# Performance work log

Measured on AMD Instinct MI355X. Metric: run time of the kernel, lower is better.

Reference implementation:

```python
import jax, jax.numpy as jnp
import numpy as np
from jax import lax

NPOINT = 1024   # num_points (FPS centroids)
RADIUS = 0.2    # ball-query radius
K = 32          # samples per ball
FILTERS = [64, 64, 128]


def setup_inputs() -> dict:
    key = jax.random.key(0)
    ks = jax.random.split(key, 10)
    B, N, C = 16, 4096, 64
    xyz = jax.random.uniform(ks[0], (B, N, 3), dtype=jnp.float32)   # unit-cube cloud
    points = jax.random.normal(ks[1], (B, N, C), dtype=jnp.float32)
    inp = {"xyz": xyz, "points": points}
    cin = C + 3  # use_xyz=True concatenates relative xyz
    for i, f in enumerate(FILTERS):
        scale = np.sqrt(2.0 / (cin + f)).astype(np.float32)  # glorot_normal
        inp[f"w{i}"] = jax.random.normal(ks[2 + i], (cin, f), dtype=jnp.float32) * scale
        inp[f"b{i}"] = jnp.zeros((f,), dtype=jnp.float32)
        cin = f
    return inp


def farthest_point_sample(xyz, npoint):
    # Serial greedy FPS. xyz: [B,N,3] -> idx [B,npoint] int32
    B, N, _ = xyz.shape

    def body(carry, _):
        dist, far = carry                                   # [B,N], [B]
        centroid = jnp.take_along_axis(xyz, far[:, None, None], axis=1)  # [B,1,3]
        d = jnp.sum((xyz - centroid) ** 2, axis=-1)         # [B,N]
        dist = jnp.minimum(dist, d)
        nxt = jnp.argmax(dist, axis=-1).astype(jnp.int32)
        return (dist, nxt), far

    init = (jnp.full((B, N), 1e10, xyz.dtype), jnp.zeros((B,), jnp.int32))
    _, idxs = lax.scan(body, init, None, length=npoint)
    return idxs.T  # [B,npoint]


def query_ball(radius, nsample, xyz, new_xyz):
    # First-nsample-in-order points within radius; pad with first hit (CUDA semantics).
    B, N, _ = xyz.shape
    d2 = jnp.sum((new_xyz[:, :, None, :] - xyz[:, None, :, :]) ** 2, axis=-1)  # [B,S,N]
    mask = d2 <= radius * radius
    order = jnp.where(mask, jnp.arange(N, dtype=jnp.int32)[None, None, :], N)
    idx_sorted = jnp.sort(order, axis=-1)[..., :nsample]    # first K valid indices
    first = idx_sorted[..., :1]
    first = jnp.where(first < N, first, 0)                  # empty-ball fallback
    return jnp.where(idx_sorted < N, idx_sorted, first)     # [B,S,K]


def reference(xyz, points, w0, b0, w1, b1, w2, b2):
    B, N, _ = xyz.shape
    fps_idx = farthest_point_sample(xyz, NPOINT)                    # [B,S]
    new_xyz = jnp.take_along_axis(xyz, fps_idx[:, :, None], axis=1)  # [B,S,3]
    idx = query_ball(RADIUS, K, xyz, new_xyz)                        # [B,S,K]

    bix = jnp.arange(B)[:, None, None]
    grouped_xyz = xyz[bix, idx] - new_xyz[:, :, None, :]             # [B,S,K,3] recentered
    grouped_pts = points[bix, idx]                                   # [B,S,K,C]
    g = jnp.concatenate([grouped_pts, grouped_xyz], axis=-1)         # [B,S,K,C+3]

    for w, b in ((w0, b0), (w1, b1), (w2, b2)):                      # shared 1x1-conv MLP
        g = jax.nn.relu(jnp.einsum('bskc,cf->bskf', g, w) + b)
    new_points = jnp.max(g, axis=2)                                  # max-pool over ball
    return new_xyz, new_points
```

## Files before the change

### kernel.cpp

```cpp
#include <hip/hip_runtime.h>
#include <stdint.h>

#define BB 16
#define NN 4096
#define CC 64
#define NPOINT 1024
#define KK 32
#define F1 64
#define F2 64
#define F3 128

#define FPS_T 512
#define PPT (NN / FPS_T)

typedef float v2f __attribute__((ext_vector_type(2)));

#if defined(__has_builtin)
#if __has_builtin(__builtin_amdgcn_update_dpp)
#define HAS_DPP 1
#endif
#endif

#ifdef HAS_DPP
template <int CTRL>
__device__ __forceinline__ unsigned long long dpp_move64(unsigned long long k) {
    int lo = __builtin_amdgcn_update_dpp(0, (int)(unsigned)k,         CTRL, 0xF, 0xF, false);
    int hi = __builtin_amdgcn_update_dpp(0, (int)(unsigned)(k >> 32), CTRL, 0xF, 0xF, false);
    return ((unsigned long long)(unsigned)hi << 32) | (unsigned)lo;
}
__device__ __forceinline__ unsigned long long wave_max_key(unsigned long long key) {
    unsigned long long o;
    o = dpp_move64<0x111>(key); if (o > key) key = o;
    o = dpp_move64<0x112>(key); if (o > key) key = o;
    o = dpp_move64<0x114>(key); if (o > key) key = o;
    o = dpp_move64<0x118>(key); if (o > key) key = o;
    o = dpp_move64<0x142>(key); if (o > key) key = o;
    o = dpp_move64<0x143>(key); if (o > key) key = o;
    return key;
}
#else
__device__ __forceinline__ unsigned long long wave_max_key(unsigned long long key) {
#pragma unroll
    for (int off = 32; off > 0; off >>= 1) {
        unsigned long long o = __shfl_xor(key, off, 64);
        if (o > key) key = o;
    }
    return key;
}
#endif

#define SMEM_BYTES 49664

__global__ __launch_bounds__(512)
void fused_kernel(const float* __restrict__ xyz,
                  const float* __restrict__ points,
                  const float* __restrict__ w0, const float* __restrict__ b0,
                  const float* __restrict__ w1, const float* __restrict__ b1,
                  const float* __restrict__ w2, const float* __restrict__ b2,
                  float* __restrict__ out_xyz,
                  float* __restrict__ out_points,
                  int* __restrict__ ctr) {
    __shared__ __align__(16) char smem[SMEM_BYTES];
    const int tid = threadIdx.x;

    if (blockIdx.x < BB) {
        asm volatile("s_setprio 3");
        float* xs = (float*)smem;
        float* ys = xs + NN;
        float* zs = ys + NN;
        unsigned long long (*wred)[FPS_T / 64] =
            (unsigned long long (*)[FPS_T / 64])(smem + 49152);
        float* cbuf = (float*)(smem + 49280);

        const int b = blockIdx.x;
        const int lane = tid & 63, wid = tid >> 6;
        const float* __restrict__ xb = xyz + (size_t)b * (NN * 3);

        v2f px2[4], py2[4], pz2[4], dd[4];
#pragma unroll
        for (int j = 0; j < 4; ++j) {
#pragma unroll
            for (int h = 0; h < 2; ++h) {
                int p = tid + (2 * j + h) * FPS_T;
                float x = xb[p * 3 + 0];
                float y = xb[p * 3 + 1];
                float z = xb[p * 3 + 2];
                px2[j][h] = x; py2[j][h] = y; pz2[j][h] = z;
                xs[p] = x; ys[p] = y; zs[p] = z;
            }
            dd[j] = (v2f){1e10f, 1e10f};
        }
        __syncthreads();

        float cx = xs[0], cy = ys[0], cz = zs[0];
        float* xo = out_xyz + (size_t)b * NPOINT * 3;

        for (int i = 0; i < NPOINT; ++i) {
            if (tid == 0) {
                cbuf[(i & 31) * 3 + 0] = cx;
                cbuf[(i & 31) * 3 + 1] = cy;
                cbuf[(i & 31) * 3 + 2] = cz;
            }
            {
#pragma clang fp contract(off)
                v2f c2x = (v2f){cx, cx}, c2y = (v2f){cy, cy}, c2z = (v2f){cz, cz};
#pragma unroll
                for (int j = 0; j < 4; ++j) {
                    v2f dx = px2[j] - c2x;
                    v2f dy = py2[j] - c2y;
                    v2f dz = pz2[j] - c2z;
                    v2f ss = (dx * dx + dy * dy) + dz * dz;
                    dd[j] = __builtin_elementwise_min(dd[j], ss);
                }
            }
            v2f m01 = __builtin_elementwise_max(dd[0], dd[1]);
            v2f m23 = __builtin_elementwise_max(dd[2], dd[3]);
            v2f mm  = __builtin_elementwise_max(m01, m23);
            float bd = fmaxf(mm.x, mm.y);
            int bp = 0;
#pragma unroll
            for (int j = 3; j >= 0; --j) {
                if (dd[j].y == bd) bp = tid + (2 * j + 1) * FPS_T;
                if (dd[j].x == bd) bp = tid + (2 * j + 0) * FPS_T;
            }
            unsigned long long key = (((unsigned long long)__float_as_uint(bd)) << 32)
                                   | (unsigned int)(NN - 1 - bp);
            key = wave_max_key(key);
            if (lane == 63) wred[i & 1][wid] = key;
            __syncthreads();

            unsigned long long best = wred[i & 1][0];
#pragma unroll
            for (int w = 1; w < FPS_T / 64; ++w) {
                unsigned long long o = wred[i & 1][w];
                if (o > best) best = o;
            }
            int bi = (NN - 1) - (int)(best & 0xffffffffu);

            if (tid == 0 && (i & 31) == 31) {
                const float4* src = (const float4*)cbuf;
                float4* dst = (float4*)(xo + (size_t)(i - 31) * 3);
#pragma unroll
                for (int q = 0; q < 24; ++q) dst[q] = src[q];
                __hip_atomic_store(&ctr[b * 16], i + 1,
                                   __ATOMIC_RELEASE, __HIP_MEMORY_SCOPE_AGENT);
            }
            cx = xs[bi]; cy = ys[bi]; cz = zs[bi];
        }
    } else {
        float (*gbuf)[68] = (float (*)[68])smem;
        float (*hbuf)[F1] = (float (*)[F1])(smem + 8704);
        float (*pmax)[F3] = (float (*)[F3])(smem + 16896);
        unsigned long long* cmask = (unsigned long long*)(smem + 20992);
        int* nbr = (int*)(smem + 21504);

        const int gi = blockIdx.x - BB;
        const int s = gi >> 4;
        const int b = gi & 15;
        const int g = b * NPOINT + s;
        const int f = tid & 63;
        const int wid = tid >> 6;

        if (tid == 0) {
            const int target = s + 1;
            int c;
            while ((c = __hip_atomic_load(&ctr[b * 16], __ATOMIC_RELAXED,
                                          __HIP_MEMORY_SCOPE_AGENT)) < target) {
                if (target - c > 64) __builtin_amdgcn_s_sleep(64);
                else                 __builtin_amdgcn_s_sleep(4);
            }
            (void)__hip_atomic_load(&ctr[b * 16], __ATOMIC_ACQUIRE,
                                    __HIP_MEMORY_SCOPE_AGENT);
        }
        __syncthreads();

        unsigned int ux = __hip_atomic_load((unsigned int*)&out_xyz[(size_t)g * 3 + 0],
                                            __ATOMIC_RELAXED, __HIP_MEMORY_SCOPE_AGENT);
        unsigned int uy = __hip_atomic_load((unsigned int*)&out_xyz[(size_t)g * 3 + 1],
                                            __ATOMIC_RELAXED, __HIP_MEMORY_SCOPE_AGENT);
        unsigned int uz = __hip_atomic_load((unsigned int*)&out_xyz[(size_t)g * 3 + 2],
                                            __ATOMIC_RELAXED, __HIP_MEMORY_SCOPE_AGENT);
        const float cx = __uint_as_float(ux);
        const float cy = __uint_as_float(uy);
        const float cz = __uint_as_float(uz);

        {
            const float* __restrict__ xb = xyz + (size_t)b * (NN * 3);
#pragma unroll
            for (int j = 0; j < 8; ++j) {
                int chunk = wid * 8 + j;
                int p = chunk * 64 + f;
                float x = xb[p * 3 + 0];
                float y = xb[p * 3 + 1];
                float z = xb[p * 3 + 2];
                float dx = __fsub_rn(cx, x);
                float dy = __fsub_rn(cy, y);
                float dz = __fsub_rn(cz, z);
                float d2 = __fadd_rn(__fadd_rn(__fmul_rn(dx, dx), __fmul_rn(dy, dy)),
                                     __fmul_rn(dz, dz));
                unsigned long long m = __ballot(d2 <= 0.04f);
                if (f == 0) cmask[chunk] = m;
            }
        }
        __syncthreads();

        if (tid < 64) {
            unsigned long long m = cmask[tid];
            int cnt = (int)__popcll(m);
            int v = cnt;
#pragma unroll
            for (int off = 1; off < 64; off <<= 1) {
                int u = __shfl_up(v, off, 64);
                if (tid >= off) v += u;
            }
            int excl = v - cnt;
            int total = __shfl(v, 63, 64);
            unsigned long long mm = m;
            int r = excl;
            while (mm && r < KK) {
                int bpos = __ffsll(mm) - 1;
                mm &= mm - 1;
                nbr[r++] = tid * 64 + bpos;
            }
            if (total < KK) {
                unsigned long long nz = __ballot(cnt > 0);
                int fchunk = __ffsll(nz) - 1;
                unsigned long long fm = cmask[fchunk];
                int first = fchunk * 64 + __ffsll(fm) - 1;
                if (tid >= total && tid < KK) nbr[tid] = first;
            }
        }
        __syncthreads();

        {
            const float* __restrict__ pb = points + (size_t)b * NN * CC;
#pragma unroll
            for (int m = 0; m < 4; ++m) {
                int k = wid + 8 * m;
                int idx = nbr[k] & (NN - 1);
                gbuf[k][f] = pb[(size_t)idx * CC + f];
            }
            if (tid < 96) {
                int k = tid & 31, q = tid >> 5;
                int idx = nbr[k] & (NN - 1);
                float v = xyz[((size_t)b * NN + idx) * 3 + q];
                float cq = (q == 0) ? cx : ((q == 1) ? cy : cz);
                gbuf[k][CC + q] = __fsub_rn(v, cq);
            }
        }
        __syncthreads();

        v2f acc2[4];

#pragma unroll
        for (int m = 0; m < 4; ++m) acc2[m] = (v2f){0.0f, 0.0f};
#pragma unroll 4
        for (int c4 = 0; c4 < 64; c4 += 4) {
            v2f wA = (v2f){w0[(c4 + 0) * F1 + f], w0[(c4 + 1) * F1 + f]};
            v2f wB = (v2f){w0[(c4 + 2) * F1 + f], w0[(c4 + 3) * F1 + f]};
#pragma unroll
            for (int m = 0; m < 4; ++m) {
                float4 gv = *(const float4*)&gbuf[wid + 8 * m][c4];
                acc2[m] = __builtin_elementwise_fma((v2f){gv.x, gv.y}, wA, acc2[m]);
                acc2[m] = __builtin_elementwise_fma((v2f){gv.z, gv.w}, wB, acc2[m]);
            }
        }
        {
            float wv0 = w0[64 * F1 + f];
            float wv1 = w0[65 * F1 + f];
            float wv2 = w0[66 * F1 + f];
            float bb = b0[f];
#pragma unroll
            for (int m = 0; m < 4; ++m) {
                int k = wid + 8 * m;
                float a = acc2[m].x + acc2[m].y;
                a = fmaf(gbuf[k][64], wv0, a);
                a = fmaf(gbuf[k][65], wv1, a);
                a = fmaf(gbuf[k][66], wv2, a);
                hbuf[k][f] = fmaxf(a + bb, 0.0f);
            }
        }
        __syncthreads();

#pragma unroll
        for (int m = 0; m < 4; ++m) acc2[m] = (v2f){0.0f, 0.0f};
#pragma unroll 4
        for (int c4 = 0; c4 < 64; c4 += 4) {
            v2f wA = (v2f){w1[(c4 + 0) * F2 + f], w1[(c4 + 1) * F2 + f]};
            v2f wB = (v2f){w1[(c4 + 2) * F2 + f], w1[(c4 + 3) * F2 + f]};
#pragma unroll
            for (int m = 0; m < 4; ++m) {
                float4 gv = *(const float4*)&hbuf[wid + 8 * m][c4];
                acc2[m] = __builtin_elementwise_fma((v2f){gv.x, gv.y}, wA, acc2[m]);
                acc2[m] = __builtin_elementwise_fma((v2f){gv.z, gv.w}, wB, acc2[m]);
            }
        }
        {
            float bb = b1[f];
#pragma unroll
            for (int m = 0; m < 4; ++m)
                gbuf[wid + 8 * m][f] = fmaxf(acc2[m].x + acc2[m].y + bb, 0.0f);
        }
        __syncthreads();

        v2f a0[4], a1[4];
#pragma unroll
        for (int m = 0; m < 4; ++m) { a0[m] = (v2f){0.f, 0.f}; a1[m] = (v2f){0.f, 0.f}; }
#pragma unroll 2
        for (int c4 = 0; c4 < 64; c4 += 4) {
            v2f wA0 = (v2f){w2[(c4 + 0) * F3 + f],      w2[(c4 + 1) * F3 + f]};
            v2f wB0 = (v2f){w2[(c4 + 2) * F3 + f],      w2[(c4 + 3) * F3 + f]};
            v2f wA1 = (v2f){w2[(c4 + 0) * F3 + f + 64], w2[(c4 + 1) * F3 + f + 64]};
            v2f wB1 = (v2f){w2[(c4 + 2) * F3 + f + 64], w2[(c4 + 3) * F3 + f + 64]};
#pragma unroll
            for (int m = 0; m < 4; ++m) {
                float4 gv = *(const float4*)&gbuf[wid + 8 * m][c4];
                a0[m] = __builtin_elementwise_fma((v2f){gv.x, gv.y}, wA0, a0[m]);
                a0[m] = __builtin_elementwise_fma((v2f){gv.z, gv.w}, wB0, a0[m]);
                a1[m] = __builtin_elementwise_fma((v2f){gv.x, gv.y}, wA1, a1[m]);
                a1[m] = __builtin_elementwise_fma((v2f){gv.z, gv.w}, wB1, a1[m]);
            }
        }
        {
            float pm0 = -1e30f, pm1 = -1e30f;
#pragma unroll
            for (int m = 0; m < 4; ++m) {
                pm0 = fmaxf(pm0, a0[m].x + a0[m].y);
                pm1 = fmaxf(pm1, a1[m].x + a1[m].y);
            }
            pmax[wid][f] = pm0;
            pmax[wid][f + 64] = pm1;
        }
        __syncthreads();
        if (tid < F3) {
            float v = pmax[0][tid];
#pragma unroll
            for (int w = 1; w < 8; ++w) v = fmaxf(v, pmax[w][tid]);
            v = fmaxf(v + b2[tid], 0.0f);
            out_points[(size_t)g * F3 + tid] = v;
        }
    }
}

extern "C" void kernel_launch(void* const* d_in, const int* in_sizes, int n_in,
                              void* d_out, int out_size, void* d_ws, size_t ws_size,
                              hipStream_t stream) {
    const float* xyz    = (const float*)d_in[0];
    const float* points = (const float*)d_in[1];
    const float* w0 = (const float*)d_in[2];
    const float* b0 = (const float*)d_in[3];
    const float* w1 = (const float*)d_in[4];
    const float* b1 = (const float*)d_in[5];
    const float* w2 = (const float*)d_in[6];
    const float* b2 = (const float*)d_in[7];

    float* out_xyz    = (float*)d_out;
    float* out_points = out_xyz + (size_t)BB * NPOINT * 3;
    int*   ctr        = (int*)d_ws;

    fused_kernel<<<BB + BB * NPOINT, 512, 0, stream>>>(
        xyz, points, w0, b0, w1, b1, w2, b2, out_xyz, out_points, ctr);
}
```

Before: 820.1 us.

## Use four FPS waves per batch and process two centroids per MLP block

The FPS blocks now run only four active waves. Each thread holds 16 points, and the other four waves idle through matching barriers, so the per-iteration cross-wave reduction is smaller. The grouping/MLP blocks each handle two centroids (64 rows), halving the number of blocks and reusing weight loads across twice as many rows. The risks are longer serial FPS arithmetic per thread, more register pressure in the MLP blocks, and consumers waiting for two centroids before starting.

```diff
diff --git a/kernel.cpp b/kernel.cpp
--- a/kernel.cpp
+++ b/kernel.cpp
@@ -10,8 +10,9 @@
 #define F2 64
 #define F3 128
 
-#define FPS_T 512
-#define PPT (NN / FPS_T)
+#define BLK_T 512
+#define FPS_ACT 256
+#define FPPT 16
 
 typedef float v2f __attribute__((ext_vector_type(2)));
 
@@ -51,7 +52,7 @@
 
 #define SMEM_BYTES 49664
 
-__global__ __launch_bounds__(512)
+__global__ __launch_bounds__(BLK_T)
 void fused_kernel(const float* __restrict__ xyz,
                   const float* __restrict__ points,
                   const float* __restrict__ w0, const float* __restrict__ b0,
@@ -65,23 +66,28 @@
 
     if (blockIdx.x < BB) {
         asm volatile("s_setprio 3");
+        const int wid8 = tid >> 6;
+        if (wid8 >= 4) {
+            for (int i = 0; i < NPOINT + 1; ++i) __syncthreads();
+            return;
+        }
         float* xs = (float*)smem;
         float* ys = xs + NN;
         float* zs = ys + NN;
-        unsigned long long (*wred)[FPS_T / 64] =
-            (unsigned long long (*)[FPS_T / 64])(smem + 49152);
+        unsigned long long (*wred)[4] =
+            (unsigned long long (*)[4])(smem + 49152);
         float* cbuf = (float*)(smem + 49280);
 
         const int b = blockIdx.x;
-        const int lane = tid & 63, wid = tid >> 6;
+        const int lane = tid & 63, wv = tid >> 6;
         const float* __restrict__ xb = xyz + (size_t)b * (NN * 3);
 
-        v2f px2[4], py2[4], pz2[4], dd[4];
-#pragma unroll
-        for (int j = 0; j < 4; ++j) {
+        v2f px2[8], py2[8], pz2[8], dd[8];
+#pragma unroll
+        for (int j = 0; j < 8; ++j) {
 #pragma unroll
             for (int h = 0; h < 2; ++h) {
-                int p = tid + (2 * j + h) * FPS_T;
+                int p = tid + (2 * j + h) * FPS_ACT;
                 float x = xb[p * 3 + 0];
                 float y = xb[p * 3 + 1];
                 float z = xb[p * 3 + 2];
@@ -105,7 +111,7 @@
 #pragma clang fp contract(off)
                 v2f c2x = (v2f){cx, cx}, c2y = (v2f){cy, cy}, c2z = (v2f){cz, cz};
 #pragma unroll
-                for (int j = 0; j < 4; ++j) {
+                for (int j = 0; j < 8; ++j) {
                     v2f dx = px2[j] - c2x;
                     v2f dy = py2[j] - c2y;
                     v2f dz = pz2[j] - c2z;
@@ -113,25 +119,29 @@
                     dd[j] = __builtin_elementwise_min(dd[j], ss);
                 }
             }
-            v2f m01 = __builtin_elementwise_max(dd[0], dd[1]);
-            v2f m23 = __builtin_elementwise_max(dd[2], dd[3]);
-            v2f mm  = __builtin_elementwise_max(m01, m23);
-            float bd = fmaxf(mm.x, mm.y);
+            v2f m0 = __builtin_elementwise_max(dd[0], dd[1]);
+            v2f m1 = __builtin_elementwise_max(dd[2], dd[3]);
+            v2f m2 = __builtin_elementwise_max(dd[4], dd[5]);
+            v2f m3 = __builtin_elementwise_max(dd[6], dd[7]);
+            m0 = __builtin_elementwise_max(m0, m1);
+            m2 = __builtin_elementwise_max(m2, m3);
+            m0 = __builtin_elementwise_max(m0, m2);
+            float bd = fmaxf(m0.x, m0.y);
             int bp = 0;
 #pragma unroll
-            for (int j = 3; j >= 0; --j) {
-                if (dd[j].y == bd) bp = tid + (2 * j + 1) * FPS_T;
-                if (dd[j].x == bd) bp = tid + (2 * j + 0) * FPS_T;
+            for (int j = 7; j >= 0; --j) {
+                if (dd[j].y == bd) bp = tid + (2 * j + 1) * FPS_ACT;
+                if (dd[j].x == bd) bp = tid + (2 * j + 0) * FPS_ACT;
             }
             unsigned long long key = (((unsigned long long)__float_as_uint(bd)) << 32)
                                    | (unsigned int)(NN - 1 - bp);
             key = wave_max_key(key);
-            if (lane == 63) wred[i & 1][wid] = key;
+            if (lane == 63) wred[i & 1][wv] = key;
             __syncthreads();
 
             unsigned long long best = wred[i & 1][0];
 #pragma unroll
-            for (int w = 1; w < FPS_T / 64; ++w) {
+            for (int w = 1; w < 4; ++w) {
                 unsigned long long o = wred[i & 1][w];
                 if (o > best) best = o;
             }
@@ -149,20 +159,21 @@
         }
     } else {
         float (*gbuf)[68] = (float (*)[68])smem;
-        float (*hbuf)[F1] = (float (*)[F1])(smem + 8704);
-        float (*pmax)[F3] = (float (*)[F3])(smem + 16896);
-        unsigned long long* cmask = (unsigned long long*)(smem + 20992);
-        int* nbr = (int*)(smem + 21504);
+        float (*hbuf)[F1] = (float (*)[F1])(smem + 17408);
+        float (*pmax)[F3] = (float (*)[F3])(smem + 33792);
+        unsigned long long* cmask = (unsigned long long*)(smem + 41984);
+        int* nbr = (int*)(smem + 43008);
 
         const int gi = blockIdx.x - BB;
-        const int s = gi >> 4;
+        const int sp = gi >> 4;
         const int b = gi & 15;
-        const int g = b * NPOINT + s;
+        const int s0 = sp * 2;
+        const int g0 = b * NPOINT + s0;
         const int f = tid & 63;
         const int wid = tid >> 6;
 
         if (tid == 0) {
-            const int target = s + 1;
+            const int target = s0 + 2;
             int c;
             while ((c = __hip_atomic_load(&ctr[b * 16], __ATOMIC_RELAXED,
                                           __HIP_MEMORY_SCOPE_AGENT)) < target) {
@@ -174,15 +185,18 @@
         }
         __syncthreads();
 
-        unsigned int ux = __hip_atomic_load((unsigned int*)&out_xyz[(size_t)g * 3 + 0],
-                                            __ATOMIC_RELAXED, __HIP_MEMORY_SCOPE_AGENT);
-        unsigned int uy = __hip_atomic_load((unsigned int*)&out_xyz[(size_t)g * 3 + 1],
-                                            __ATOMIC_RELAXED, __HIP_MEMORY_SCOPE_AGENT);
-        unsigned int uz = __hip_atomic_load((unsigned int*)&out_xyz[(size_t)g * 3 + 2],
-                                            __ATOMIC_RELAXED, __HIP_MEMORY_SCOPE_AGENT);
-        const float cx = __uint_as_float(ux);
-        const float cy = __uint_as_float(uy);
-        const float cz = __uint_as_float(uz);
+        float cen[2][3];
+#pragma unroll
+        for (int grp = 0; grp < 2; ++grp)
+#pragma unroll
+            for (int q = 0; q < 3; ++q) {
+                unsigned int u = __hip_atomic_load(
+                    (unsigned int*)&out_xyz[(size_t)(g0 + grp) * 3 + q],
+                    __ATOMIC_RELAXED, __HIP_MEMORY_SCOPE_AGENT);
+                cen[grp][q] = __uint_as_float(u);
+            }
+        const float cx0 = cen[0][0], cy0 = cen[0][1], cz0 = cen[0][2];
+        const float cx1 = cen[1][0], cy1 = cen[1][1], cz1 = cen[1][2];
 
         {
             const float* __restrict__ xb = xyz + (size_t)b * (NN * 3);
@@ -193,25 +207,28 @@
                 float x = xb[p * 3 + 0];
                 float y = xb[p * 3 + 1];
                 float z = xb[p * 3 + 2];
-                float dx = __fsub_rn(cx, x);
-                float dy = __fsub_rn(cy, y);
-                float dz = __fsub_rn(cz, z);
-                float d2 = __fadd_rn(__fadd_rn(__fmul_rn(dx, dx), __fmul_rn(dy, dy)),
-                                     __fmul_rn(dz, dz));
-                unsigned long long m = __ballot(d2 <= 0.04f);
-                if (f == 0) cmask[chunk] = m;
-            }
-        }
-        __syncthreads();
-
-        if (tid < 64) {
-            unsigned long long m = cmask[tid];
+                float dx0 = __fsub_rn(cx0, x), dy0 = __fsub_rn(cy0, y), dz0 = __fsub_rn(cz0, z);
+                float d20 = __fadd_rn(__fadd_rn(__fmul_rn(dx0, dx0), __fmul_rn(dy0, dy0)),
+                                      __fmul_rn(dz0, dz0));
+                float dx1 = __fsub_rn(cx1, x), dy1 = __fsub_rn(cy1, y), dz1 = __fsub_rn(cz1, z);
+                float d21 = __fadd_rn(__fadd_rn(__fmul_rn(dx1, dx1), __fmul_rn(dy1, dy1)),
+                                      __fmul_rn(dz1, dz1));
+                unsigned long long m0 = __ballot(d20 <= 0.04f);
+                unsigned long long m1 = __ballot(d21 <= 0.04f);
+                if (f == 0) { cmask[chunk] = m0; cmask[64 + chunk] = m1; }
+            }
+        }
+        __syncthreads();
+
+        if (tid < 128) {
+            const int grp = wid;
+            unsigned long long m = cmask[grp * 64 + f];
             int cnt = (int)__popcll(m);
             int v = cnt;
 #pragma unroll
             for (int off = 1; off < 64; off <<= 1) {
                 int u = __shfl_up(v, off, 64);
-                if (tid >= off) v += u;
+                if (f >= off) v += u;
             }
             int excl = v - cnt;
             int total = __shfl(v, 63, 64);
@@ -220,14 +237,14 @@
             while (mm && r < KK) {
                 int bpos = __ffsll(mm) - 1;
                 mm &= mm - 1;
-                nbr[r++] = tid * 64 + bpos;
+                nbr[grp * 32 + (r++)] = f * 64 + bpos;
             }
             if (total < KK) {
                 unsigned long long nz = __ballot(cnt > 0);
                 int fchunk = __ffsll(nz) - 1;
-                unsigned long long fm = cmask[fchunk];
+                unsigned long long fm = cmask[grp * 64 + fchunk];
                 int first = fchunk * 64 + __ffsll(fm) - 1;
-                if (tid >= total && tid < KK) nbr[tid] = first;
+                if (f >= total && f < KK) nbr[grp * 32 + f] = first;
             }
         }
         __syncthreads();
@@ -235,31 +252,32 @@
         {
             const float* __restrict__ pb = points + (size_t)b * NN * CC;
 #pragma unroll
-            for (int m = 0; m < 4; ++m) {
-                int k = wid + 8 * m;
-                int idx = nbr[k] & (NN - 1);
-                gbuf[k][f] = pb[(size_t)idx * CC + f];
-            }
-            if (tid < 96) {
-                int k = tid & 31, q = tid >> 5;
-                int idx = nbr[k] & (NN - 1);
+            for (int m = 0; m < 8; ++m) {
+                int r = wid + 8 * m;
+                int grp = r >> 5, k = r & 31;
+                int idx = nbr[grp * 32 + k] & (NN - 1);
+                gbuf[r][f] = pb[(size_t)idx * CC + f];
+            }
+            if (tid < 192) {
+                int r = tid & 63, q = tid >> 6;
+                int grp = r >> 5, k = r & 31;
+                int idx = nbr[grp * 32 + k] & (NN - 1);
                 float v = xyz[((size_t)b * NN + idx) * 3 + q];
-                float cq = (q == 0) ? cx : ((q == 1) ? cy : cz);
-                gbuf[k][CC + q] = __fsub_rn(v, cq);
-            }
-        }
-        __syncthreads();
-
-        v2f acc2[4];
-
-#pragma unroll
-        for (int m = 0; m < 4; ++m) acc2[m] = (v2f){0.0f, 0.0f};
+                gbuf[r][CC + q] = __fsub_rn(v, cen[grp][q]);
+            }
+        }
+        __syncthreads();
+
+        v2f acc2[8];
+
+#pragma unroll
+        for (int m = 0; m < 8; ++m) acc2[m] = (v2f){0.0f, 0.0f};
 #pragma unroll 4
         for (int c4 = 0; c4 < 64; c4 += 4) {
             v2f wA = (v2f){w0[(c4 + 0) * F1 + f], w0[(c4 + 1) * F1 + f]};
             v2f wB = (v2f){w0[(c4 + 2) * F1 + f], w0[(c4 + 3) * F1 + f]};
 #pragma unroll
-            for (int m = 0; m < 4; ++m) {
+            for (int m = 0; m < 8; ++m) {
                 float4 gv = *(const float4*)&gbuf[wid + 8 * m][c4];
                 acc2[m] = __builtin_elementwise_fma((v2f){gv.x, gv.y}, wA, acc2[m]);
                 acc2[m] = __builtin_elementwise_fma((v2f){gv.z, gv.w}, wB, acc2[m]);
@@ -271,25 +289,25 @@
             float wv2 = w0[66 * F1 + f];
             float bb = b0[f];
 #pragma unroll
-            for (int m = 0; m < 4; ++m) {
-                int k = wid + 8 * m;
+            for (int m = 0; m < 8; ++m) {
+                int r = wid + 8 * m;
                 float a = acc2[m].x + acc2[m].y;
-                a = fmaf(gbuf[k][64], wv0, a);
-                a = fmaf(gbuf[k][65], wv1, a);
-                a = fmaf(gbuf[k][66], wv2, a);
-                hbuf[k][f] = fmaxf(a + bb, 0.0f);
-            }
-        }
-        __syncthreads();
-
-#pragma unroll
-        for (int m = 0; m < 4; ++m) acc2[m] = (v2f){0.0f, 0.0f};
+                a = fmaf(gbuf[r][64], wv0, a);
+                a = fmaf(gbuf[r][65], wv1, a);
+                a = fmaf(gbuf[r][66], wv2, a);
+                hbuf[r][f] = fmaxf(a + bb, 0.0f);
+            }
+        }
+        __syncthreads();
+
+#pragma unroll
+        for (int m = 0; m < 8; ++m) acc2[m] = (v2f){0.0f, 0.0f};
 #pragma unroll 4
         for (int c4 = 0; c4 < 64; c4 += 4) {
             v2f wA = (v2f){w1[(c4 + 0) * F2 + f], w1[(c4 + 1) * F2 + f]};
             v2f wB = (v2f){w1[(c4 + 2) * F2 + f], w1[(c4 + 3) * F2 + f]};
 #pragma unroll
-            for (int m = 0; m < 4; ++m) {
+            for (int m = 0; m < 8; ++m) {
                 float4 gv = *(const float4*)&hbuf[wid + 8 * m][c4];
                 acc2[m] = __builtin_elementwise_fma((v2f){gv.x, gv.y}, wA, acc2[m]);
                 acc2[m] = __builtin_elementwise_fma((v2f){gv.z, gv.w}, wB, acc2[m]);
@@ -298,46 +316,44 @@
         {
             float bb = b1[f];
 #pragma unroll
-            for (int m = 0; m < 4; ++m)
+            for (int m = 0; m < 8; ++m)
                 gbuf[wid + 8 * m][f] = fmaxf(acc2[m].x + acc2[m].y + bb, 0.0f);
         }
         __syncthreads();
 
-        v2f a0[4], a1[4];
-#pragma unroll
-        for (int m = 0; m < 4; ++m) { a0[m] = (v2f){0.f, 0.f}; a1[m] = (v2f){0.f, 0.f}; }
-#pragma unroll 2
-        for (int c4 = 0; c4 < 64; c4 += 4) {
-            v2f wA0 = (v2f){w2[(c4 + 0) * F3 + f],      w2[(c4 + 1) * F3 + f]};
-            v2f wB0 = (v2f){w2[(c4 + 2) * F3 + f],      w2[(c4 + 3) * F3 + f]};
-            v2f wA1 = (v2f){w2[(c4 + 0) * F3 + f + 64], w2[(c4 + 1) * F3 + f + 64]};
-            v2f wB1 = (v2f){w2[(c4 + 2) * F3 + f + 64], w2[(c4 + 3) * F3 + f + 64]};
-#pragma unroll
-            for (int m = 0; m < 4; ++m) {
-                float4 gv = *(const float4*)&gbuf[wid + 8 * m][c4];
-                a0[m] = __builtin_elementwise_fma((v2f){gv.x, gv.y}, wA0, a0[m]);
-                a0[m] = __builtin_elementwise_fma((v2f){gv.z, gv.w}, wB0, a0[m]);
-                a1[m] = __builtin_elementwise_fma((v2f){gv.x, gv.y}, wA1, a1[m]);
-                a1[m] = __builtin_elementwise_fma((v2f){gv.z, gv.w}, wB1, a1[m]);
-            }
-        }
-        {
-            float pm0 = -1e30f, pm1 = -1e30f;
-#pragma unroll
-            for (int m = 0; m < 4; ++m) {
-                pm0 = fmaxf(pm0, a0[m].x + a0[m].y);
-                pm1 = fmaxf(pm1, a1[m].x + a1[m].y);
-            }
-            pmax[wid][f] = pm0;
-            pmax[wid][f + 64] = pm1;
-        }
-        __syncthreads();
-        if (tid < F3) {
-            float v = pmax[0][tid];
-#pragma unroll
-            for (int w = 1; w < 8; ++w) v = fmaxf(v, pmax[w][tid]);
-            v = fmaxf(v + b2[tid], 0.0f);
-            out_points[(size_t)g * F3 + tid] = v;
+#pragma unroll
+        for (int h = 0; h < 2; ++h) {
+#pragma unroll
+            for (int m = 0; m < 8; ++m) acc2[m] = (v2f){0.0f, 0.0f};
+#pragma unroll 4
+            for (int c4 = 0; c4 < 64; c4 += 4) {
+                v2f wA = (v2f){w2[(c4 + 0) * F3 + 64 * h + f], w2[(c4 + 1) * F3 + 64 * h + f]};
+                v2f wB = (v2f){w2[(c4 + 2) * F3 + 64 * h + f], w2[(c4 + 3) * F3 + 64 * h + f]};
+#pragma unroll
+                for (int m = 0; m < 8; ++m) {
+                    float4 gv = *(const float4*)&gbuf[wid + 8 * m][c4];
+                    acc2[m] = __builtin_elementwise_fma((v2f){gv.x, gv.y}, wA, acc2[m]);
+                    acc2[m] = __builtin_elementwise_fma((v2f){gv.z, gv.w}, wB, acc2[m]);
+                }
+            }
+            {
+                float pm0 = -1e30f, pm1 = -1e30f;
+#pragma unroll
+                for (int m = 0; m < 4; ++m) pm0 = fmaxf(pm0, acc2[m].x + acc2[m].y);
+#pragma unroll
+                for (int m = 4; m < 8; ++m) pm1 = fmaxf(pm1, acc2[m].x + acc2[m].y);
+                pmax[wid][64 * h + f] = pm0;
+                pmax[8 + wid][64 * h + f] = pm1;
+            }
+        }
+        __syncthreads();
+        if (tid < 256) {
+            int grp = tid >> 7, c = tid & 127;
+            float v = pmax[grp * 8][c];
+#pragma unroll
+            for (int w = 1; w < 8; ++w) v = fmaxf(v, pmax[grp * 8 + w][c]);
+            v = fmaxf(v + b2[c], 0.0f);
+            out_points[(size_t)(g0 + grp) * F3 + c] = v;
         }
     }
 }
@@ -358,6 +374,6 @@
     float* out_points = out_xyz + (size_t)BB * NPOINT * 3;
     int*   ctr        = (int*)d_ws;
 
-    fused_kernel<<<BB + BB * NPOINT, 512, 0, stream>>>(
+    fused_kernel<<<BB + BB * NPOINT / 2, BLK_T, 0, stream>>>(
         xyz, points, w0, b0, w1, b1, w2, b2, out_xyz, out_points, ctr);
 }
```

New measurement: 961.3 us. 17.2% more time.
